# Performance work log

Hardware: AMD Instinct MI355X
Metric: run time of the kernel (lower is better)

The kernel has to match this reference:

```python
import jax, jax.numpy as jnp
import numpy as np

BATCH = 32
NUM_VARS = 16
SAMPLES = 4096
EMBED_DIM = 128
WINDOW_SIZE = 32
STEP_SIZE = 4
WIDTH = 1.0


def setup_inputs() -> dict:
    key = jax.random.key(0)
    k1, k2, k3, k4, k5 = jax.random.split(key, 5)
    x = jax.random.normal(k1, (BATCH, NUM_VARS, SAMPLES), dtype=jnp.float32)
    # sample-level LSH: num_variables -> embed_dim
    W_sample = jax.random.normal(k2, (NUM_VARS, EMBED_DIM), dtype=jnp.float32)
    b_sample = jax.random.uniform(k3, (EMBED_DIM,), dtype=jnp.float32, minval=0.0, maxval=WIDTH)
    # patch-level LSH: window_size*embed_dim -> embed_dim
    W_patch = jax.random.normal(k4, (WINDOW_SIZE * EMBED_DIM, EMBED_DIM), dtype=jnp.float32)
    b_patch = jax.random.uniform(k5, (EMBED_DIM,), dtype=jnp.float32, minval=0.0, maxval=WIDTH)
    return {"x": x, "W_sample": W_sample, "b_sample": b_sample,
            "W_patch": W_patch, "b_patch": b_patch}


def reference(x, W_sample, b_sample, W_patch, b_patch):
    batch, v, samples = x.shape
    # encode: E2LSH hash of every timestep, fully vectorized over the samples axis
    # enc: [B, S, D]
    enc = jnp.floor((jnp.einsum('bvs,vd->bsd', x, W_sample) + b_sample) / WIDTH)
    # quantize: sliding windows over time, flattened then hashed
    num_tokens = (samples - WINDOW_SIZE) // STEP_SIZE  # matches preallocated tokens
    # idx: [T, W] gather indices for all windows at once
    idx = jnp.arange(num_tokens)[:, None] * STEP_SIZE + jnp.arange(WINDOW_SIZE)[None, :]
    windows = enc[:, idx, :].reshape(batch, num_tokens, WINDOW_SIZE * EMBED_DIM)  # [B, T, W*D]
    tokens = jnp.floor((windows @ W_patch + b_patch) / WIDTH)  # [B, T, D]
    return tokens
```

## Files before the change

kernel.cpp:

```cpp
#include <hip/hip_runtime.h>
#include <hip/hip_bf16.h>
#include <cstdint>

#define BATCH   32
#define NVARS   16
#define SAMPLES 4096
#define EDIM    128
#define NTOK    1016

typedef __bf16 bf8_t __attribute__((ext_vector_type(8)));
typedef float  f4_t  __attribute__((ext_vector_type(4)));

__global__ __launch_bounds__(256) void prep_kernel(
    const float* __restrict__ Wp, __hip_bfloat16* __restrict__ WtF)
{
  __shared__ float ls[32][132];
  int tid = threadIdx.x;
  int kb  = blockIdx.x;
  int s = kb >> 3, dlt = kb & 7;
  int kbase = (4 * dlt + (s & 3)) * 128 + (s >> 2) * 32;
#pragma unroll
  for (int r = 0; r < 16; ++r) {
    int idx = tid + r * 256;
    ls[idx >> 7][idx & 127] =
        Wp[(size_t)(kbase + (idx >> 7)) * EDIM + (idx & 127)];
  }
  __syncthreads();
  int g = tid >> 5, l5 = tid & 31;
#pragma unroll
  for (int h = 0; h < 2; ++h) {
    int lane = l5 + h * 32;
    int quad = lane >> 4, l15 = lane & 15;
    int n = g * 16 + l15;
    union { unsigned short u[8]; uint4 v; } pk;
#pragma unroll
    for (int t = 0; t < 8; ++t) {
      __hip_bfloat16 hh = __float2bfloat16(ls[quad * 8 + t][n]);
      pk.u[t] = *(unsigned short*)&hh;
    }
    *(uint4*)(WtF + (size_t)kb * 4096 + g * 512 + lane * 8) = pk.v;
  }
}

__global__ __launch_bounds__(512, 2) void gemm_kernel(
    const float* __restrict__ x,
    const float* __restrict__ Ws,
    const float* __restrict__ bs,
    const __hip_bfloat16* __restrict__ WtF,
    const float* __restrict__ bp,
    float* __restrict__ out)
{
  __shared__ __align__(16) __hip_bfloat16 Apl[2][2][4608];
  __shared__ __align__(16) float xT[4][136][20];

  int tid  = threadIdx.x;
  int lane = tid & 63;
  int wv   = tid >> 6;
  int g    = wv >> 2;
  int wq   = wv & 3;
  int b    = blockIdx.x >> 3;
  int t0   = (blockIdx.x & 7) << 7;
  int wm   = (wq >> 1) << 6;
  int wn   = (wq & 1) << 6;
  int quad = lane >> 4;
  int l15  = lane & 15;

  const __hip_bfloat16* bg = WtF + (size_t)(wn >> 4) * 512 + lane * 8;

  f4_t acc[4][4];
  f4_t zero = {0.f, 0.f, 0.f, 0.f};
#pragma unroll
  for (int i = 0; i < 4; ++i)
#pragma unroll
    for (int j = 0; j < 4; ++j) acc[i][j] = zero;

  {
    int v = tid >> 5, l5 = tid & 31;
    const float* xb = x + ((size_t)b * NVARS + v) * SAMPLES;
    int sb = t0 << 2;
#pragma unroll
    for (int j = 0; j < 17; ++j) {
      int i = l5 + j * 32;
      int s = sb + i; s = s > (SAMPLES - 1) ? (SAMPLES - 1) : s;
      xT[i & 3][i >> 2][v] = xb[s];
    }
  }

  float w[NVARS][4];
  float bz[4];
  auto loadW = [&](int e) {
    int d0 = e * 32 + (tid & 7) * 4;
#pragma unroll
    for (int v = 0; v < NVARS; ++v)
      *(float4*)&w[v][0] = *(const float4*)(Ws + v * EDIM + d0);
    *(float4*)&bz[0] = *(const float4*)(bs + d0);
  };
  loadW(g * 2);

  auto encU = [&](int Pg, int buf, int k) {
    int gt = tid & 255;
    if (k == 4 && gt >= 64) return;
    int p  = Pg & 3;
    int r0 = gt >> 3;
    int r  = (k < 4) ? (r0 + k * 32) : (128 + r0);
    int h  = tid & 7;
    const float* xrow = &xT[p][r][0];
    float xr[NVARS];
    *(float4*)&xr[0]  = *(const float4*)(xrow + 0);
    *(float4*)&xr[4]  = *(const float4*)(xrow + 4);
    *(float4*)&xr[8]  = *(const float4*)(xrow + 8);
    *(float4*)&xr[12] = *(const float4*)(xrow + 12);
    float a0 = bz[0], a1 = bz[1], a2 = bz[2], a3 = bz[3];
#pragma unroll
    for (int v = 0; v < NVARS; ++v) {
      a0 += xr[v] * w[v][0]; a1 += xr[v] * w[v][1];
      a2 += xr[v] * w[v][2]; a3 += xr[v] * w[v][3];
    }
    int u    = t0 + r;
    int phys = ((h >> 1) + (u >> 1)) & 3;
    union { unsigned short us[4]; uint2 q; } pk;
    pk.us[0] = (unsigned short)(__float_as_uint(floorf(a0)) >> 16);
    pk.us[1] = (unsigned short)(__float_as_uint(floorf(a1)) >> 16);
    pk.us[2] = (unsigned short)(__float_as_uint(floorf(a2)) >> 16);
    pk.us[3] = (unsigned short)(__float_as_uint(floorf(a3)) >> 16);
    *(uint2*)(&Apl[g][buf][0] + (size_t)r * 32 + phys * 8 + (h & 1) * 4) =
        pk.q;
  };

  auto loadB = [&](int kb, uint4* d) {
#pragma unroll
    for (int j = 0; j < 4; ++j)
      d[j] = *(const uint4*)(bg + (size_t)kb * 4096 + j * 512);
  };

  auto compute = [&](int abuf, int dlt, const uint4* bq_) {
    const bf8_t* pA = (const bf8_t*)&Apl[g][abuf][0];
    int swzA = (quad + ((t0 + dlt + wm + l15) >> 1)) & 3;
    bf8_t af[4];
#pragma unroll
    for (int i = 0; i < 4; ++i)
      af[i] = pA[(dlt + wm + i * 16 + l15) * 4 + swzA];
    __builtin_amdgcn_s_setprio(1);
#pragma unroll
    for (int mi = 0; mi < 4; ++mi)
#pragma unroll
      for (int ni = 0; ni < 4; ++ni)
        acc[mi][ni] = __builtin_amdgcn_mfma_f32_16x16x32_bf16(
            af[mi], __builtin_bit_cast(bf8_t, bq_[ni]), acc[mi][ni], 0, 0, 0);
    __builtin_amdgcn_s_setprio(0);
  };

  __syncthreads();
#pragma unroll
  for (int k = 0; k < 5; ++k) encU(g * 8, 0, k);
  asm volatile("s_waitcnt lgkmcnt(0)" ::: "memory");
  asm volatile("s_barrier" ::: "memory");

  uint4 bq[2][4];
  loadB(g * 64, bq[0]);
  loadB(g * 64 + 1, bq[1]);

  for (int ss = 0; ss < 8; ++ss) {
    if (ss == 3) loadW(g * 2 + 1);
#pragma unroll
    for (int d = 0; d < 8; ++d) {
      int kl = ss * 8 + d;
      compute(ss & 1, d, bq[d & 1]);
      if (kl < 62) loadB(g * 64 + kl + 2, bq[d & 1]);
      if (ss < 7 && d < 5) encU(g * 8 + ss + 1, (ss + 1) & 1, d);
    }
    asm volatile("s_waitcnt lgkmcnt(0)" ::: "memory");
    asm volatile("s_barrier" ::: "memory");
  }

  float* rb = (float*)&Apl[0][0][0];
  int widx = (wq * 64 + lane) * 17;
  float bias[4];
#pragma unroll
  for (int ni = 0; ni < 4; ++ni) bias[ni] = bp[wn + ni * 16 + l15];

#pragma unroll
  for (int mi = 0; mi < 4; ++mi) {
    __syncthreads();
    if (g == 1) {
#pragma unroll
      for (int ni = 0; ni < 4; ++ni)
#pragma unroll
        for (int r = 0; r < 4; ++r)
          rb[widx + ni * 4 + r] = acc[mi][ni][r];
    }
    __syncthreads();
    if (g == 0) {
#pragma unroll
      for (int ni = 0; ni < 4; ++ni)
#pragma unroll
        for (int r = 0; r < 4; ++r) {
          int t = t0 + wm + mi * 16 + quad * 4 + r;
          if (t < NTOK) {
            int n = wn + ni * 16 + l15;
            out[((size_t)b * NTOK + t) * EDIM + n] =
                floorf(acc[mi][ni][r] + rb[widx + ni * 4 + r] + bias[ni]);
          }
        }
    }
  }
}

extern "C" void kernel_launch(void* const* d_in, const int* in_sizes, int n_in,
                              void* d_out, int out_size, void* d_ws, size_t ws_size,
                              hipStream_t stream) {
  const float* x  = (const float*)d_in[0];
  const float* Ws = (const float*)d_in[1];
  const float* bs = (const float*)d_in[2];
  const float* Wp = (const float*)d_in[3];
  const float* bp = (const float*)d_in[4];
  float* out = (float*)d_out;

  __hip_bfloat16* WtF = (__hip_bfloat16*)d_ws;

  prep_kernel<<<128, 256, 0, stream>>>(Wp, WtF);
  gemm_kernel<<<BATCH * 8, 512, 0, stream>>>(x, Ws, bs, WtF, bp, out);
}
```

Measured before the change: 125.0 us.

## Precompute full encoded A panel in LDS before barrier-free MFMA loop

Instead of interleaving sample encoding with the MFMA loop in a double-buffered A panel with per-stage barriers, the kernel now encodes all 16 panels (4 phases x 4 embed chunks) up front into a large LDS buffer. Then the GEMM loop runs with no barriers. x is loaded with vectorized float4 reads into registers and staged per phase. LDS grows to about 140KB, which forces one block per CU (launch bounds 1), trading occupancy and encode/compute overlap for fewer syncs.

```diff
diff --git a/kernel.cpp b/kernel.cpp
--- a/kernel.cpp
+++ b/kernel.cpp
@@ -7,6 +7,7 @@
 #define SAMPLES 4096
 #define EDIM    128
 #define NTOK    1016
+#define PLELEM  4368
 
 typedef __bf16 bf8_t __attribute__((ext_vector_type(8)));
 typedef float  f4_t  __attribute__((ext_vector_type(4)));
@@ -42,7 +43,7 @@
   }
 }
 
-__global__ __launch_bounds__(512, 2) void gemm_kernel(
+__global__ __launch_bounds__(512, 1) void fused_kernel(
     const float* __restrict__ x,
     const float* __restrict__ Ws,
     const float* __restrict__ bs,
@@ -50,8 +51,8 @@
     const float* __restrict__ bp,
     float* __restrict__ out)
 {
-  __shared__ __align__(16) __hip_bfloat16 Apl[2][2][4608];
-  __shared__ __align__(16) float xT[4][136][20];
+  __shared__ __align__(16) __hip_bfloat16 Apan[16 * PLELEM];
+  __shared__ __align__(16) float xTp[2][136][16];
 
   int tid  = threadIdx.x;
   int lane = tid & 63;
@@ -67,65 +68,93 @@
 
   const __hip_bfloat16* bg = WtF + (size_t)(wn >> 4) * 512 + lane * 8;
 
-  f4_t acc[4][4];
-  f4_t zero = {0.f, 0.f, 0.f, 0.f};
-#pragma unroll
-  for (int i = 0; i < 4; ++i)
-#pragma unroll
-    for (int j = 0; j < 4; ++j) acc[i][j] = zero;
-
-  {
-    int v = tid >> 5, l5 = tid & 31;
-    const float* xb = x + ((size_t)b * NVARS + v) * SAMPLES;
-    int sb = t0 << 2;
-#pragma unroll
-    for (int j = 0; j < 17; ++j) {
-      int i = l5 + j * 32;
-      int s = sb + i; s = s > (SAMPLES - 1) ? (SAMPLES - 1) : s;
-      xT[i & 3][i >> 2][v] = xb[s];
-    }
-  }
+  int q4 = tid & 31;
+  int eq = q4 >> 3;
+  int cq = (q4 >> 1) & 3;
+  int hq = q4 & 1;
+  int r0 = tid >> 5;
 
   float w[NVARS][4];
   float bz[4];
-  auto loadW = [&](int e) {
-    int d0 = e * 32 + (tid & 7) * 4;
+  {
+    int d0 = q4 * 4;
 #pragma unroll
     for (int v = 0; v < NVARS; ++v)
       *(float4*)&w[v][0] = *(const float4*)(Ws + v * EDIM + d0);
     *(float4*)&bz[0] = *(const float4*)(bs + d0);
-  };
-  loadW(g * 2);
-
-  auto encU = [&](int Pg, int buf, int k) {
-    int gt = tid & 255;
-    if (k == 4 && gt >= 64) return;
-    int p  = Pg & 3;
-    int r0 = gt >> 3;
-    int r  = (k < 4) ? (r0 + k * 32) : (128 + r0);
-    int h  = tid & 7;
-    const float* xrow = &xT[p][r][0];
-    float xr[NVARS];
-    *(float4*)&xr[0]  = *(const float4*)(xrow + 0);
-    *(float4*)&xr[4]  = *(const float4*)(xrow + 4);
-    *(float4*)&xr[8]  = *(const float4*)(xrow + 8);
-    *(float4*)&xr[12] = *(const float4*)(xrow + 12);
+  }
+
+  int vv = tid & 15, rr = tid >> 4;
+  float4 xreg[5];
+  {
+    const float* xb = x + ((size_t)b * NVARS + vv) * SAMPLES;
+#pragma unroll
+    for (int j = 0; j < 4; ++j) {
+      int s4 = (t0 + rr + 32 * j) * 4;
+      xreg[j] = *(const float4*)(xb + s4);
+    }
+    if (tid < 128) {
+      int s4 = (t0 + 128 + rr) * 4;
+      if (s4 > SAMPLES - 4) s4 = SAMPLES - 4;
+      xreg[4] = *(const float4*)(xb + s4);
+    }
+  }
+
+  auto stageX = [&](int p, int buf) {
+#pragma unroll
+    for (int j = 0; j < 4; ++j) {
+      float c = (p == 0) ? xreg[j].x : (p == 1) ? xreg[j].y
+              : (p == 2) ? xreg[j].z : xreg[j].w;
+      xTp[buf][rr + 32 * j][vv] = c;
+    }
+    if (tid < 128) {
+      float c = (p == 0) ? xreg[4].x : (p == 1) ? xreg[4].y
+              : (p == 2) ? xreg[4].z : xreg[4].w;
+      xTp[buf][128 + rr][vv] = c;
+    }
+  };
+
+  auto encTask = [&](int p, int buf, int r) {
+    const float* xr = &xTp[buf][r][0];
+    float xv[NVARS];
+    *(float4*)&xv[0]  = *(const float4*)(xr + 0);
+    *(float4*)&xv[4]  = *(const float4*)(xr + 4);
+    *(float4*)&xv[8]  = *(const float4*)(xr + 8);
+    *(float4*)&xv[12] = *(const float4*)(xr + 12);
     float a0 = bz[0], a1 = bz[1], a2 = bz[2], a3 = bz[3];
 #pragma unroll
     for (int v = 0; v < NVARS; ++v) {
-      a0 += xr[v] * w[v][0]; a1 += xr[v] * w[v][1];
-      a2 += xr[v] * w[v][2]; a3 += xr[v] * w[v][3];
-    }
-    int u    = t0 + r;
-    int phys = ((h >> 1) + (u >> 1)) & 3;
+      a0 += xv[v] * w[v][0]; a1 += xv[v] * w[v][1];
+      a2 += xv[v] * w[v][2]; a3 += xv[v] * w[v][3];
+    }
     union { unsigned short us[4]; uint2 q; } pk;
     pk.us[0] = (unsigned short)(__float_as_uint(floorf(a0)) >> 16);
     pk.us[1] = (unsigned short)(__float_as_uint(floorf(a1)) >> 16);
     pk.us[2] = (unsigned short)(__float_as_uint(floorf(a2)) >> 16);
     pk.us[3] = (unsigned short)(__float_as_uint(floorf(a3)) >> 16);
-    *(uint2*)(&Apl[g][buf][0] + (size_t)r * 32 + phys * 8 + (h & 1) * 4) =
-        pk.q;
-  };
+    int phys = (cq + (r >> 1)) & 3;
+    char* plbase = (char*)&Apan[(eq * 4 + p) * PLELEM];
+    *(uint2*)(plbase + r * 64 + phys * 16 + hq * 8) = pk.q;
+  };
+
+  stageX(0, 0);
+  __syncthreads();
+#pragma unroll
+  for (int p = 0; p < 4; ++p) {
+    if (p < 3) stageX(p + 1, (p + 1) & 1);
+    int buf = p & 1;
+#pragma unroll
+    for (int j = 0; j < 8; ++j) encTask(p, buf, r0 + 16 * j);
+    if (tid < 256) encTask(p, buf, 128 + (tid >> 5));
+    __syncthreads();
+  }
+
+  f4_t acc[4][4];
+  f4_t zero = {0.f, 0.f, 0.f, 0.f};
+#pragma unroll
+  for (int i = 0; i < 4; ++i)
+#pragma unroll
+    for (int j = 0; j < 4; ++j) acc[i][j] = zero;
 
   auto loadB = [&](int kb, uint4* d) {
 #pragma unroll
@@ -133,8 +162,7 @@
       d[j] = *(const uint4*)(bg + (size_t)kb * 4096 + j * 512);
   };
 
-  auto compute = [&](int abuf, int dlt, const uint4* bq_) {
-    const bf8_t* pA = (const bf8_t*)&Apl[g][abuf][0];
+  auto compute = [&](const bf8_t* pA, int dlt, const uint4* bq_) {
     int swzA = (quad + ((t0 + dlt + wm + l15) >> 1)) & 3;
     bf8_t af[4];
 #pragma unroll
@@ -150,30 +178,22 @@
     __builtin_amdgcn_s_setprio(0);
   };
 
-  __syncthreads();
-#pragma unroll
-  for (int k = 0; k < 5; ++k) encU(g * 8, 0, k);
-  asm volatile("s_waitcnt lgkmcnt(0)" ::: "memory");
-  asm volatile("s_barrier" ::: "memory");
-
   uint4 bq[2][4];
   loadB(g * 64, bq[0]);
   loadB(g * 64 + 1, bq[1]);
 
   for (int ss = 0; ss < 8; ++ss) {
-    if (ss == 3) loadW(g * 2 + 1);
+    int pl = (g * 2 + (ss >> 2)) * 4 + (ss & 3);
+    const bf8_t* pA = (const bf8_t*)&Apan[pl * PLELEM];
 #pragma unroll
     for (int d = 0; d < 8; ++d) {
       int kl = ss * 8 + d;
-      compute(ss & 1, d, bq[d & 1]);
+      compute(pA, d, bq[d & 1]);
       if (kl < 62) loadB(g * 64 + kl + 2, bq[d & 1]);
-      if (ss < 7 && d < 5) encU(g * 8 + ss + 1, (ss + 1) & 1, d);
-    }
-    asm volatile("s_waitcnt lgkmcnt(0)" ::: "memory");
-    asm volatile("s_barrier" ::: "memory");
-  }
-
-  float* rb = (float*)&Apl[0][0][0];
+    }
+  }
+
+  float* rb = (float*)&Apan[0];
   int widx = (wq * 64 + lane) * 17;
   float bias[4];
 #pragma unroll
@@ -219,5 +239,5 @@
   __hip_bfloat16* WtF = (__hip_bfloat16*)d_ws;
 
   prep_kernel<<<128, 256, 0, stream>>>(Wp, WtF);
-  gemm_kernel<<<BATCH * 8, 512, 0, stream>>>(x, Ws, bs, WtF, bp, out);
+  fused_kernel<<<BATCH * 8, 512, 0, stream>>>(x, Ws, bs, WtF, bp, out);
 }
```

New measurement: 106.7 us. 1.17x faster.
